# Optimization experiments

Measured on AMD Instinct MI355X. Metric: run time of the kernel, lower is better.

## Reference

```python
import jax, jax.numpy as jnp
import numpy as np
from jax.ops import segment_sum

N_NODES = 50000
N_EDGES = 800000
IN_DIM, HID_DIM, OUT_DIM = 128, 128, 64
N_GRAPHS = 64


def setup_inputs() -> dict:
    key = jax.random.key(0)
    ks = jax.random.split(key, 8)
    x = jax.random.normal(ks[0], (N_NODES, IN_DIM), dtype=jnp.float32)
    edge_index = jax.random.randint(ks[1], (2, N_EDGES), 0, N_NODES, dtype=jnp.int64)
    batch = jnp.sort(jax.random.randint(ks[2], (N_NODES,), 0, N_GRAPHS, dtype=jnp.int64))
    # Glorot-ish init for GCNConv linear weights, zero bias (PyG default)
    W1 = jax.random.normal(ks[3], (IN_DIM, HID_DIM), dtype=jnp.float32) / np.sqrt(IN_DIM)
    b1 = jnp.zeros((HID_DIM,), dtype=jnp.float32)
    W2 = jax.random.normal(ks[4], (HID_DIM, OUT_DIM), dtype=jnp.float32) / np.sqrt(HID_DIM)
    b2 = jnp.zeros((OUT_DIM,), dtype=jnp.float32)
    return {"x": x, "W1": W1, "b1": b1, "W2": W2, "b2": b2,
            "edge_index": edge_index, "batch": batch, "num_graphs": N_GRAPHS}


def _gcn_conv(h, W, b, src, dst, deg_inv_sqrt, n_nodes):
    # h: [N, Fin] -> [N, Fout]; GCNConv: D^{-1/2}(A+I)D^{-1/2} (h W) + b
    hw = h @ W                                   # [N, Fout]
    norm = deg_inv_sqrt[src] * deg_inv_sqrt[dst] # [E]
    msg = hw[src] * norm[:, None]                # [E, Fout] (gather)
    agg = segment_sum(msg, dst, num_segments=n_nodes)  # scatter-add
    # self-loop contribution: norm_ii = deg_inv_sqrt[i]^2
    agg = agg + hw * (deg_inv_sqrt * deg_inv_sqrt)[:, None]
    return agg + b


def reference(x, W1, b1, W2, b2, edge_index, batch, num_graphs):
    n_nodes = x.shape[0]
    src, dst = edge_index[0], edge_index[1]
    # degree of A + I (self-loops added, as in PyG GCNConv default)
    deg = segment_sum(jnp.ones_like(dst, dtype=x.dtype), dst,
                      num_segments=n_nodes) + 1.0
    deg_inv_sqrt = jax.lax.rsqrt(deg)

    h = jax.nn.relu(_gcn_conv(x, W1, b1, src, dst, deg_inv_sqrt, n_nodes))
    h = jax.nn.relu(_gcn_conv(h, W2, b2, src, dst, deg_inv_sqrt, n_nodes))

    # global_mean_pool over batch ids
    sums = segment_sum(h, batch, num_segments=num_graphs)          # [G, Fout]
    counts = segment_sum(jnp.ones((n_nodes,), dtype=h.dtype), batch,
                         num_segments=num_graphs)                  # [G]
    return sums / jnp.maximum(counts, 1.0)[:, None]
```

## Files before the change

### kernel.cpp

```cpp
#include <hip/hip_runtime.h>

typedef float f4 __attribute__((ext_vector_type(4)));
typedef float f2 __attribute__((ext_vector_type(2)));
typedef short s8 __attribute__((ext_vector_type(8)));

union FU { unsigned u[4]; s8 s; };

__device__ __forceinline__ unsigned cvtpk(float lo, float hi){
  unsigned r;
  asm("v_cvt_pk_bf16_f32 %0, %1, %2" : "=v"(r) : "v"(lo), "v"(hi));
  return r;
}

__device__ __forceinline__ float bflo(unsigned v){ return __uint_as_float(v << 16); }
__device__ __forceinline__ float bfhi(unsigned v){ return __uint_as_float(v & 0xFFFF0000u); }

__device__ __forceinline__ int ld_idx(const void* p, int i, int is64){
  if (is64) return (int)((const long long*)p)[i];
  return ((const int*)p)[i];
}

__device__ __forceinline__ int detect64(const unsigned* __restrict__ e_raw, int e){
  int lane = threadIdx.x & 63;
  int lim = (e < 1024) ? e : 1024;
  int nz = 0;
  for (int i = lane; i < lim; i += 64) nz |= (e_raw[2*i + 1] != 0u);
  return (__ballot(nz != 0) == 0ull) ? 1 : 0;
}

template<int NC, int BIN>
__device__ __forceinline__ void gemm_body(const void* __restrict__ Xv,
                                          const float* __restrict__ W,
                                          unsigned short* __restrict__ Yb,
                                          int n, int blk, char* Alds){
  constexpr int NCF = NC/16;
  constexpr int WPC = 8/NCF;
  constexpr int RT  = 8/WPC;
  const int tid  = threadIdx.x;
  const int wave = tid >> 6, lane = tid & 63;
  const int rb = blk * 128;

  const int cbase = (wave % NCF) * 16;
  const int rt0   = (wave / NCF) * RT;
  const int col   = cbase + (lane & 15);
  const int kr0   = (lane >> 4) * 8;
  FU bu[4];
#pragma unroll
  for (int ks = 0; ks < 4; ++ks){
    float wv[8];
#pragma unroll
    for (int j = 0; j < 8; ++j) wv[j] = W[(size_t)(ks*32 + kr0 + j)*NC + col];
#pragma unroll
    for (int q = 0; q < 4; ++q) bu[ks].u[q] = cvtpk(wv[2*q], wv[2*q+1]);
  }

  for (int i = tid; i < 128*32; i += 512){
    int row = i >> 5, kq = i & 31;
    int rsrc = rb + row; if (rsrc >= n) rsrc = n - 1;
    uint2 dw;
    if (BIN){
      dw = ((const uint2*)Xv)[(size_t)rsrc*32 + kq];
    } else {
      f4 xv = ((const f4*)Xv)[(size_t)rsrc*32 + kq];
      dw = make_uint2(cvtpk(xv[0], xv[1]), cvtpk(xv[2], xv[3]));
    }
    int byte = (row*256 + kq*8) ^ ((row & 7) << 4);
    *reinterpret_cast<uint2*>(Alds + byte) = dw;
  }
  __syncthreads();

  f4 acc[RT];
#pragma unroll
  for (int rt = 0; rt < RT; ++rt) acc[rt] = 0.0f;

#pragma unroll
  for (int rt = 0; rt < RT; ++rt){
    const int arow = (rt0 + rt)*16 + (lane & 15);
#pragma unroll
    for (int ks = 0; ks < 4; ++ks){
      int kb = ks*32 + kr0;
      int byte = (arow*256 + kb*2) ^ ((arow & 7) << 4);
      s8 a = *reinterpret_cast<const s8*>(Alds + byte);
      acc[rt] = __builtin_amdgcn_mfma_f32_16x16x32_bf16(a, bu[ks].s, acc[rt], 0, 0, 0);
    }
  }

#pragma unroll
  for (int rt = 0; rt < RT; ++rt){
    int rowb = rb + (rt0 + rt)*16 + 4*(lane >> 4);
#pragma unroll
    for (int r = 0; r < 4; ++r){
      int row = rowb + r;
      if (row < n) Yb[(size_t)row*NC + col] = (unsigned short)cvtpk(acc[rt][r], acc[rt][r]);
    }
  }
}

template<int NC, int BIN>
__global__ __launch_bounds__(512) void gemm_k(const void* __restrict__ X,
                                              const float* __restrict__ W,
                                              unsigned short* __restrict__ Yb, int n){
  __shared__ int4 AldsV[2048];
  gemm_body<NC, BIN>(X, W, Yb, n, blockIdx.x, (char*)AldsV);
}

__global__ __launch_bounds__(512) void fused1_k(const float* __restrict__ X,
                                                const float* __restrict__ W1,
                                                unsigned short* __restrict__ Yb,
                                                const void* __restrict__ eidx,
                                                const void* __restrict__ batchp,
                                                int* __restrict__ counts,
                                                unsigned* __restrict__ etmp,
                                                int* __restrict__ batch32,
                                                int n, int e, int GB, int CB){
  __shared__ int4 AldsV[2048];
  __shared__ int hist[512];
  int blk = blockIdx.x;
  if (blk < GB){
    gemm_body<128, 0>(X, W1, Yb, n, blk, (char*)AldsV);
    return;
  }
  blk -= GB;
  const int NBK = (n + 127) >> 7;
  for (int i = threadIdx.x; i < NBK; i += 512) hist[i] = 0;
  __syncthreads();
  int is64 = detect64((const unsigned*)eidx, e);
  int CHK = (e + CB - 1) / CB;
  int beg = blk*CHK, end = min(e, beg + CHK);
  for (int i = beg + (int)threadIdx.x; i < end; i += 512){
    int s = ld_idx(eidx, i, is64);
    int d = ld_idx(eidx, e + i, is64);
    atomicAdd(&hist[d >> 7], 1);
    etmp[i] = (unsigned)s | ((unsigned)(d & 127) << 16) | ((unsigned)(d >> 7) << 23);
  }
  __syncthreads();
  for (int i = threadIdx.x; i < NBK; i += 512) counts[i*CB + blk] = hist[i];
  for (int i = blk*512 + (int)threadIdx.x; i < n; i += CB*512)
    batch32[i] = ld_idx(batchp, i, is64);
}

__global__ void scanA_k(const int* __restrict__ counts, int* __restrict__ base,
                        int* __restrict__ bsum, int L,
                        float* __restrict__ outsum, int totalOut){
  __shared__ int sh[256];
  int tid = threadIdx.x;
  int i = blockIdx.x*256 + tid;
  int v = (i < L) ? counts[i] : 0;
  sh[tid] = v; __syncthreads();
  for (int off = 1; off < 256; off <<= 1){
    int t = (tid >= off) ? sh[tid - off] : 0;
    __syncthreads();
    sh[tid] += t;
    __syncthreads();
  }
  if (i < L) base[i] = sh[tid] - v;
  if (tid == 255) bsum[blockIdx.x] = sh[255];
  if (blockIdx.x == 0){
    for (int k = tid; k < totalOut; k += 256) outsum[k] = 0.0f;
  }
}

__global__ __launch_bounds__(512) void scat_k(const unsigned* __restrict__ etmp,
                                              const int* __restrict__ base,
                                              const int* __restrict__ bsum,
                                              int* __restrict__ bsumS,
                                              int* __restrict__ packed,
                                              int n, int e, int CB){
  __shared__ int sh[512];
  __shared__ int cur[512];
  int blk = blockIdx.x, tid = threadIdx.x;
  const int NBK = (n + 127) >> 7;
  int v = (tid < NBK) ? bsum[tid] : 0;
  sh[tid] = v; __syncthreads();
  for (int o = 1; o < 512; o <<= 1){
    int t = (tid >= o) ? sh[tid - o] : 0;
    __syncthreads();
    sh[tid] += t;
    __syncthreads();
  }
  int ex = sh[tid] - v;
  if (tid < NBK) cur[tid] = ex + base[tid*CB + blk];
  if (blk == 0){
    if (tid < NBK) bsumS[tid] = ex;
    if (tid == NBK - 1) bsumS[NBK] = sh[tid];
  }
  __syncthreads();
  int CHK = (e + CB - 1) / CB;
  int beg = blk*CHK, end = min(e, beg + CHK);
  for (int i = beg + tid; i < end; i += 512){
    unsigned w = etmp[i];
    int pos = atomicAdd(&cur[w >> 23], 1);
    packed[pos] = (int)(w & 0x7FFFFFu);
  }
}

#define CSR_CAP 6144
__global__ __launch_bounds__(256) void csr_k(const int* __restrict__ packed,
                                             const int* __restrict__ bsumS,
                                             int* __restrict__ esrcS,
                                             int* __restrict__ rowptr,
                                             float* __restrict__ dinv, int n, int e){
  __shared__ int vals[CSR_CAP];
  __shared__ int hist[128], off[128], cur[128];
  int b = blockIdx.x, tid = threadIdx.x;
  if (b == 0 && tid == 0) rowptr[n] = e;
  int sbeg = bsumS[b], send = bsumS[b + 1];
  int m = send - sbeg;
  int mL = min(m, CSR_CAP);
  for (int i = tid; i < mL; i += 256) vals[i] = packed[sbeg + i];
  if (tid < 128) hist[tid] = 0;
  __syncthreads();
  for (int i = tid; i < m; i += 256){
    int v = (i < CSR_CAP) ? vals[i] : packed[sbeg + i];
    atomicAdd(&hist[(v >> 16) & 127], 1);
  }
  __syncthreads();
  if (tid < 128) off[tid] = hist[tid];
  __syncthreads();
  for (int o = 1; o < 128; o <<= 1){
    int v = 0;
    if (tid < 128 && tid >= o) v = off[tid - o];
    __syncthreads();
    if (tid < 128) off[tid] += v;
    __syncthreads();
  }
  if (tid < 128){
    int ex = off[tid] - hist[tid];
    cur[tid] = ex;
    int node = b*128 + tid;
    if (node < n){
      rowptr[node] = sbeg + ex;
      dinv[node] = rsqrtf((float)hist[tid] + 1.0f);
    }
  }
  __syncthreads();
  for (int i = tid; i < m; i += 256){
    int v = (i < CSR_CAP) ? vals[i] : packed[sbeg + i];
    int pos = atomicAdd(&cur[(v >> 16) & 127], 1);
    esrcS[sbeg + pos] = v & 0xFFFF;
  }
}

__global__ __launch_bounds__(256) void agg128_k(const unsigned short* __restrict__ HWb,
                                                const float* __restrict__ dinv,
                                                const int* __restrict__ rowptr,
                                                const int* __restrict__ esrcS,
                                                const float* __restrict__ bias,
                                                unsigned* __restrict__ Hb, int n){
  int wid  = (blockIdx.x*256 + threadIdx.x) >> 6;
  int lane = threadIdx.x & 63;
  if (wid >= n) return;
  wid = __builtin_amdgcn_readfirstlane(wid);
  float di = dinv[wid];
  float di2 = di * di;
  int beg = __builtin_amdgcn_readfirstlane(rowptr[wid]);
  int end = __builtin_amdgcn_readfirstlane(rowptr[wid + 1]);
  unsigned sv = ((const unsigned*)(HWb + (size_t)wid*128))[lane];
  float a0 = bflo(sv) * di2, a1 = bfhi(sv) * di2;
  int j = beg;
  for (; j + 16 <= end; j += 16){
    int s[16]; float dv[16]; unsigned v[16];
#pragma unroll
    for (int t = 0; t < 16; ++t) s[t] = esrcS[j + t];
#pragma unroll
    for (int t = 0; t < 16; ++t){
      dv[t] = dinv[s[t]];
      v[t] = ((const unsigned*)(HWb + (size_t)s[t]*128))[lane];
    }
#pragma unroll
    for (int t = 0; t < 16; ++t){
      float wt = dv[t] * di;
      a0 += bflo(v[t]) * wt;
      a1 += bfhi(v[t]) * wt;
    }
  }
  for (; j + 4 <= end; j += 4){
    int s[4]; float dv[4]; unsigned v[4];
#pragma unroll
    for (int t = 0; t < 4; ++t) s[t] = esrcS[j + t];
#pragma unroll
    for (int t = 0; t < 4; ++t){
      dv[t] = dinv[s[t]];
      v[t] = ((const unsigned*)(HWb + (size_t)s[t]*128))[lane];
    }
#pragma unroll
    for (int t = 0; t < 4; ++t){
      float wt = dv[t] * di;
      a0 += bflo(v[t]) * wt;
      a1 += bfhi(v[t]) * wt;
    }
  }
  for (; j < end; ++j){
    int s = esrcS[j];
    float wt = dinv[s] * di;
    unsigned v = ((const unsigned*)(HWb + (size_t)s*128))[lane];
    a0 += bflo(v) * wt;
    a1 += bfhi(v) * wt;
  }
  f2 bb = ((const f2*)bias)[lane];
  a0 = fmaxf(a0 + bb[0], 0.0f);
  a1 = fmaxf(a1 + bb[1], 0.0f);
  Hb[(size_t)wid*64 + lane] = cvtpk(a0, a1);
}

__global__ __launch_bounds__(256) void agg64_k(const unsigned short* __restrict__ HWb,
                                               const float* __restrict__ dinv,
                                               const int* __restrict__ rowptr,
                                               const int* __restrict__ esrcS,
                                               const float* __restrict__ bias,
                                               float* __restrict__ H2, int n){
  int wid  = (blockIdx.x*256 + threadIdx.x) >> 6;
  int lane = threadIdx.x & 63;
  if (wid >= n) return;
  wid = __builtin_amdgcn_readfirstlane(wid);
  float di = dinv[wid];
  float di2 = di * di;
  int beg = __builtin_amdgcn_readfirstlane(rowptr[wid]);
  int end = __builtin_amdgcn_readfirstlane(rowptr[wid + 1]);
  float acc = bflo((unsigned)HWb[(size_t)wid*64 + lane]) * di2;
  int j = beg;
  for (; j + 16 <= end; j += 16){
    int s[16]; float dv[16]; unsigned v[16];
#pragma unroll
    for (int t = 0; t < 16; ++t) s[t] = esrcS[j + t];
#pragma unroll
    for (int t = 0; t < 16; ++t){
      dv[t] = dinv[s[t]];
      v[t] = (unsigned)HWb[(size_t)s[t]*64 + lane];
    }
#pragma unroll
    for (int t = 0; t < 16; ++t) acc += bflo(v[t]) * (dv[t] * di);
  }
  for (; j + 4 <= end; j += 4){
    int s[4]; float dv[4]; unsigned v[4];
#pragma unroll
    for (int t = 0; t < 4; ++t) s[t] = esrcS[j + t];
#pragma unroll
    for (int t = 0; t < 4; ++t){
      dv[t] = dinv[s[t]];
      v[t] = (unsigned)HWb[(size_t)s[t]*64 + lane];
    }
#pragma unroll
    for (int t = 0; t < 4; ++t) acc += bflo(v[t]) * (dv[t] * di);
  }
  for (; j < end; ++j){
    int s = esrcS[j];
    acc += bflo((unsigned)HWb[(size_t)s*64 + lane]) * (dinv[s] * di);
  }
  acc = fmaxf(acc + bias[lane], 0.0f);
  H2[(size_t)wid*64 + lane] = acc;
}

__global__ __launch_bounds__(256) void pool_k(const float* __restrict__ H2,
                                              const int* __restrict__ batch32,
                                              float* __restrict__ outsum, int n){
  int wid  = (blockIdx.x*256 + threadIdx.x) >> 6;
  int lane = threadIdx.x & 63;
  int start = wid * 8;
  if (start >= n) return;
  int cnt = min(8, n - start);
  float v[8]; int b[8];
#pragma unroll
  for (int t = 0; t < 8; ++t){
    int i = start + t; if (i >= n) i = n - 1;
    v[t] = H2[(size_t)i*64 + lane];
    b[t] = batch32[i];
  }
  float acc = 0.0f;
  int gcur = b[0];
#pragma unroll
  for (int t = 0; t < 8; ++t){
    if (t < cnt){
      if (b[t] != gcur){
        unsafeAtomicAdd(&outsum[gcur*64 + lane], acc);
        acc = 0.0f; gcur = b[t];
      }
      acc += v[t];
    }
  }
  unsafeAtomicAdd(&outsum[gcur*64 + lane], acc);
}

__global__ void fin_k(const float* __restrict__ outsum,
                      const int* __restrict__ batch32,
                      float* __restrict__ out, int n, int g){
  __shared__ int starts[257];
  int t = threadIdx.x;
  if (t <= g){
    int lo = 0, hi = n;
    while (lo < hi){ int mid = (lo + hi) >> 1; if (batch32[mid] < t) lo = mid + 1; else hi = mid; }
    starts[t] = lo;
  }
  __syncthreads();
  for (int idx = t; idx < (g << 6); idx += 256){
    int gi = idx >> 6;
    float c = (float)(starts[gi + 1] - starts[gi]);
    out[idx] = outsum[idx] / fmaxf(c, 1.0f);
  }
}

extern "C" void kernel_launch(void* const* d_in, const int* in_sizes, int n_in,
                              void* d_out, int out_size, void* d_ws, size_t ws_size,
                              hipStream_t stream){
  const float* x    = (const float*)d_in[0];
  const float* W1   = (const float*)d_in[1];
  const float* b1   = (const float*)d_in[2];
  const float* W2   = (const float*)d_in[3];
  const float* b2   = (const float*)d_in[4];
  const void*  eidx = d_in[5];
  const void*  batchp = d_in[6];
  const int n = in_sizes[0] / 128;
  const int e = in_sizes[5] / 2;
  const int g = out_size / 64;
  float* out = (float*)d_out;

  const int NBK = (n + 127) >> 7;
  const int CB  = 256;
  const int GB  = (n + 127) / 128;
  const int L   = NBK * CB;

  char* w = (char*)d_ws;
  int* counts  = (int*)w;
  int* base    = counts + (size_t)L;
  int* bsum    = base + (size_t)L;
  int* bsumS   = bsum + NBK;
  int* rowptr  = bsumS + (NBK + 1);
  int* batch32 = rowptr + (n + 1);
  float* dinv  = (float*)(batch32 + n);
  float* outsum = dinv + n;
  unsigned* etmp = (unsigned*)(outsum + out_size);
  int* packed  = (int*)(etmp + e);
  int* esrcS   = packed + e;
  size_t ofs = (size_t)((char*)(esrcS + e) - w);
  ofs = (ofs + 255) & ~(size_t)255;
  unsigned short* HWb = (unsigned short*)(w + ofs);
  size_t ofs2 = ofs + (size_t)n * 128 * 2;
  ofs2 = (ofs2 + 255) & ~(size_t)255;
  unsigned short* Hb = (unsigned short*)(w + ofs2);
  size_t ofs3 = ofs2 + (size_t)n * 128 * 2;
  ofs3 = (ofs3 + 255) & ~(size_t)255;
  float* H2 = (float*)(w + ofs3);

  fused1_k<<<GB + CB, 512, 0, stream>>>(x, W1, HWb, eidx, batchp,
                                        counts, etmp, batch32, n, e, GB, CB);
  scanA_k<<<NBK, 256, 0, stream>>>(counts, base, bsum, L, outsum, out_size);
  scat_k<<<CB, 512, 0, stream>>>(etmp, base, bsum, bsumS, packed, n, e, CB);
  csr_k<<<NBK, 256, 0, stream>>>(packed, bsumS, esrcS, rowptr, dinv, n, e);

  agg128_k<<<(n + 3)/4, 256, 0, stream>>>(HWb, dinv, rowptr, esrcS, b1,
                                          (unsigned*)Hb, n);
  gemm_k<64, 1><<<GB, 512, 0, stream>>>(Hb, W2, HWb, n);
  agg64_k<<<(n + 3)/4, 256, 0, stream>>>(HWb, dinv, rowptr, esrcS, b2, H2, n);

  int pw = (n + 7)/8;
  pool_k<<<(pw + 3)/4, 256, 0, stream>>>(H2, batch32, outsum, n);
  fin_k<<<1, 256, 0, stream>>>(outsum, batch32, out, n, g);
}
```

Baseline: 120.2 us.

## Vectorize neighbor gathers with per-lane edge slots and fold mean-pool finalize

The aggregation kernels now split each wavefront into edge slots (4 slots of 16 lanes for width 128, 8 slots of 8 lanes for width 64). Each lane loads 16 bytes of a neighbor row, so several edges are gathered at once, and the partial sums are combined with cross-lane shuffles at the end. This replaces narrow per-lane 4- or 2-byte gathers and is meant to increase memory-level parallelism and cut the number of load instructions per edge. Separately, the per-graph inverse counts are computed in scanA_k, and pool_k atomically adds scaled values straight into the output, which removes the fin_k launch and the outsum buffer. The costs are shuffle reductions, idle lanes when degrees are small, and float atomics on the output with a different summation order.

```diff
diff --git a/kernel.cpp b/kernel.cpp
--- a/kernel.cpp
+++ b/kernel.cpp
@@ -141,8 +141,10 @@
 
 __global__ void scanA_k(const int* __restrict__ counts, int* __restrict__ base,
                         int* __restrict__ bsum, int L,
-                        float* __restrict__ outsum, int totalOut){
+                        const int* __restrict__ batch32, float* __restrict__ invc,
+                        float* __restrict__ out, int n, int g){
   __shared__ int sh[256];
+  __shared__ int starts[257];
   int tid = threadIdx.x;
   int i = blockIdx.x*256 + tid;
   int v = (i < L) ? counts[i] : 0;
@@ -156,7 +158,17 @@
   if (i < L) base[i] = sh[tid] - v;
   if (tid == 255) bsum[blockIdx.x] = sh[255];
   if (blockIdx.x == 0){
-    for (int k = tid; k < totalOut; k += 256) outsum[k] = 0.0f;
+    if (tid <= g){
+      int lo = 0, hi = n;
+      while (lo < hi){ int mid = (lo + hi) >> 1; if (batch32[mid] < tid) lo = mid + 1; else hi = mid; }
+      starts[tid] = lo;
+    }
+    __syncthreads();
+    if (tid < g){
+      float c = (float)(starts[tid + 1] - starts[tid]);
+      invc[tid] = 1.0f / fmaxf(c, 1.0f);
+    }
+    for (int k = tid; k < (g << 6); k += 256) out[k] = 0.0f;
   }
 }
 
@@ -246,61 +258,73 @@
                                                 const int* __restrict__ rowptr,
                                                 const int* __restrict__ esrcS,
                                                 const float* __restrict__ bias,
-                                                unsigned* __restrict__ Hb, int n){
+                                                unsigned short* __restrict__ Hb, int n){
   int wid  = (blockIdx.x*256 + threadIdx.x) >> 6;
   int lane = threadIdx.x & 63;
   if (wid >= n) return;
   wid = __builtin_amdgcn_readfirstlane(wid);
+  const int slot = lane >> 4;
+  const int cg   = lane & 15;
   float di = dinv[wid];
   float di2 = di * di;
   int beg = __builtin_amdgcn_readfirstlane(rowptr[wid]);
   int end = __builtin_amdgcn_readfirstlane(rowptr[wid + 1]);
-  unsigned sv = ((const unsigned*)(HWb + (size_t)wid*128))[lane];
-  float a0 = bflo(sv) * di2, a1 = bfhi(sv) * di2;
+  float acc[8];
+#pragma unroll
+  for (int k = 0; k < 8; ++k) acc[k] = 0.0f;
+  const char* Hc = (const char*)HWb;
   int j = beg;
   for (; j + 16 <= end; j += 16){
-    int s[16]; float dv[16]; unsigned v[16];
-#pragma unroll
-    for (int t = 0; t < 16; ++t) s[t] = esrcS[j + t];
-#pragma unroll
-    for (int t = 0; t < 16; ++t){
-      dv[t] = dinv[s[t]];
-      v[t] = ((const unsigned*)(HWb + (size_t)s[t]*128))[lane];
-    }
-#pragma unroll
-    for (int t = 0; t < 16; ++t){
-      float wt = dv[t] * di;
-      a0 += bflo(v[t]) * wt;
-      a1 += bfhi(v[t]) * wt;
-    }
-  }
-  for (; j + 4 <= end; j += 4){
-    int s[4]; float dv[4]; unsigned v[4];
-#pragma unroll
-    for (int t = 0; t < 4; ++t) s[t] = esrcS[j + t];
-#pragma unroll
-    for (int t = 0; t < 4; ++t){
-      dv[t] = dinv[s[t]];
-      v[t] = ((const unsigned*)(HWb + (size_t)s[t]*128))[lane];
-    }
-#pragma unroll
-    for (int t = 0; t < 4; ++t){
-      float wt = dv[t] * di;
-      a0 += bflo(v[t]) * wt;
-      a1 += bfhi(v[t]) * wt;
-    }
-  }
-  for (; j < end; ++j){
-    int s = esrcS[j];
-    float wt = dinv[s] * di;
-    unsigned v = ((const unsigned*)(HWb + (size_t)s*128))[lane];
-    a0 += bflo(v) * wt;
-    a1 += bfhi(v) * wt;
-  }
-  f2 bb = ((const f2*)bias)[lane];
-  a0 = fmaxf(a0 + bb[0], 0.0f);
-  a1 = fmaxf(a1 + bb[1], 0.0f);
-  Hb[(size_t)wid*64 + lane] = cvtpk(a0, a1);
+    int s[4]; float wt[4]; uint4 v[4];
+#pragma unroll
+    for (int q = 0; q < 4; ++q) s[q] = esrcS[j + q*4 + slot];
+#pragma unroll
+    for (int q = 0; q < 4; ++q){
+      wt[q] = dinv[s[q]] * di;
+      v[q] = *(const uint4*)(Hc + (size_t)s[q]*256 + cg*16);
+    }
+#pragma unroll
+    for (int q = 0; q < 4; ++q){
+      acc[0] += bflo(v[q].x)*wt[q]; acc[1] += bfhi(v[q].x)*wt[q];
+      acc[2] += bflo(v[q].y)*wt[q]; acc[3] += bfhi(v[q].y)*wt[q];
+      acc[4] += bflo(v[q].z)*wt[q]; acc[5] += bfhi(v[q].z)*wt[q];
+      acc[6] += bflo(v[q].w)*wt[q]; acc[7] += bfhi(v[q].w)*wt[q];
+    }
+  }
+  for (; j < end; j += 4){
+    int idx = j + slot;
+    int live = (idx < end);
+    if (!live) idx = end - 1;
+    int s = esrcS[idx];
+    float wt = live ? (dinv[s] * di) : 0.0f;
+    uint4 v = *(const uint4*)(Hc + (size_t)s*256 + cg*16);
+    acc[0] += bflo(v.x)*wt; acc[1] += bfhi(v.x)*wt;
+    acc[2] += bflo(v.y)*wt; acc[3] += bfhi(v.y)*wt;
+    acc[4] += bflo(v.z)*wt; acc[5] += bfhi(v.z)*wt;
+    acc[6] += bflo(v.w)*wt; acc[7] += bfhi(v.w)*wt;
+  }
+#pragma unroll
+  for (int k = 0; k < 8; ++k){
+    acc[k] += __shfl_xor(acc[k], 16);
+    acc[k] += __shfl_xor(acc[k], 32);
+  }
+  uint4 sv = *(const uint4*)(Hc + (size_t)wid*256 + cg*16);
+  acc[0] += bflo(sv.x)*di2; acc[1] += bfhi(sv.x)*di2;
+  acc[2] += bflo(sv.y)*di2; acc[3] += bfhi(sv.y)*di2;
+  acc[4] += bflo(sv.z)*di2; acc[5] += bfhi(sv.z)*di2;
+  acc[6] += bflo(sv.w)*di2; acc[7] += bfhi(sv.w)*di2;
+  f4 b0 = *(const f4*)(bias + cg*8);
+  f4 b1 = *(const f4*)(bias + cg*8 + 4);
+#pragma unroll
+  for (int k = 0; k < 4; ++k) acc[k] = fmaxf(acc[k] + b0[k], 0.0f);
+#pragma unroll
+  for (int k = 0; k < 4; ++k) acc[4+k] = fmaxf(acc[4+k] + b1[k], 0.0f);
+  if (slot == 0){
+    uint4 o;
+    o.x = cvtpk(acc[0], acc[1]); o.y = cvtpk(acc[2], acc[3]);
+    o.z = cvtpk(acc[4], acc[5]); o.w = cvtpk(acc[6], acc[7]);
+    *(uint4*)((char*)Hb + (size_t)wid*256 + cg*16) = o;
+  }
 }
 
 __global__ __launch_bounds__(256) void agg64_k(const unsigned short* __restrict__ HWb,
@@ -313,47 +337,75 @@
   int lane = threadIdx.x & 63;
   if (wid >= n) return;
   wid = __builtin_amdgcn_readfirstlane(wid);
+  const int slot = lane >> 3;
+  const int cg   = lane & 7;
   float di = dinv[wid];
   float di2 = di * di;
   int beg = __builtin_amdgcn_readfirstlane(rowptr[wid]);
   int end = __builtin_amdgcn_readfirstlane(rowptr[wid + 1]);
-  float acc = bflo((unsigned)HWb[(size_t)wid*64 + lane]) * di2;
+  float acc[8];
+#pragma unroll
+  for (int k = 0; k < 8; ++k) acc[k] = 0.0f;
+  const char* Hc = (const char*)HWb;
   int j = beg;
   for (; j + 16 <= end; j += 16){
-    int s[16]; float dv[16]; unsigned v[16];
-#pragma unroll
-    for (int t = 0; t < 16; ++t) s[t] = esrcS[j + t];
-#pragma unroll
-    for (int t = 0; t < 16; ++t){
-      dv[t] = dinv[s[t]];
-      v[t] = (unsigned)HWb[(size_t)s[t]*64 + lane];
-    }
-#pragma unroll
-    for (int t = 0; t < 16; ++t) acc += bflo(v[t]) * (dv[t] * di);
-  }
-  for (; j + 4 <= end; j += 4){
-    int s[4]; float dv[4]; unsigned v[4];
-#pragma unroll
-    for (int t = 0; t < 4; ++t) s[t] = esrcS[j + t];
-#pragma unroll
-    for (int t = 0; t < 4; ++t){
-      dv[t] = dinv[s[t]];
-      v[t] = (unsigned)HWb[(size_t)s[t]*64 + lane];
-    }
-#pragma unroll
-    for (int t = 0; t < 4; ++t) acc += bflo(v[t]) * (dv[t] * di);
-  }
-  for (; j < end; ++j){
-    int s = esrcS[j];
-    acc += bflo((unsigned)HWb[(size_t)s*64 + lane]) * (dinv[s] * di);
-  }
-  acc = fmaxf(acc + bias[lane], 0.0f);
-  H2[(size_t)wid*64 + lane] = acc;
+    int s[2]; float wt[2]; uint4 v[2];
+#pragma unroll
+    for (int q = 0; q < 2; ++q) s[q] = esrcS[j + q*8 + slot];
+#pragma unroll
+    for (int q = 0; q < 2; ++q){
+      wt[q] = dinv[s[q]] * di;
+      v[q] = *(const uint4*)(Hc + (size_t)s[q]*128 + cg*16);
+    }
+#pragma unroll
+    for (int q = 0; q < 2; ++q){
+      acc[0] += bflo(v[q].x)*wt[q]; acc[1] += bfhi(v[q].x)*wt[q];
+      acc[2] += bflo(v[q].y)*wt[q]; acc[3] += bfhi(v[q].y)*wt[q];
+      acc[4] += bflo(v[q].z)*wt[q]; acc[5] += bfhi(v[q].z)*wt[q];
+      acc[6] += bflo(v[q].w)*wt[q]; acc[7] += bfhi(v[q].w)*wt[q];
+    }
+  }
+  for (; j < end; j += 8){
+    int idx = j + slot;
+    int live = (idx < end);
+    if (!live) idx = end - 1;
+    int s = esrcS[idx];
+    float wt = live ? (dinv[s] * di) : 0.0f;
+    uint4 v = *(const uint4*)(Hc + (size_t)s*128 + cg*16);
+    acc[0] += bflo(v.x)*wt; acc[1] += bfhi(v.x)*wt;
+    acc[2] += bflo(v.y)*wt; acc[3] += bfhi(v.y)*wt;
+    acc[4] += bflo(v.z)*wt; acc[5] += bfhi(v.z)*wt;
+    acc[6] += bflo(v.w)*wt; acc[7] += bfhi(v.w)*wt;
+  }
+#pragma unroll
+  for (int k = 0; k < 8; ++k){
+    acc[k] += __shfl_xor(acc[k], 8);
+    acc[k] += __shfl_xor(acc[k], 16);
+    acc[k] += __shfl_xor(acc[k], 32);
+  }
+  uint4 sv = *(const uint4*)(Hc + (size_t)wid*128 + cg*16);
+  acc[0] += bflo(sv.x)*di2; acc[1] += bfhi(sv.x)*di2;
+  acc[2] += bflo(sv.y)*di2; acc[3] += bfhi(sv.y)*di2;
+  acc[4] += bflo(sv.z)*di2; acc[5] += bfhi(sv.z)*di2;
+  acc[6] += bflo(sv.w)*di2; acc[7] += bfhi(sv.w)*di2;
+  f4 b0 = *(const f4*)(bias + cg*8);
+  f4 b1 = *(const f4*)(bias + cg*8 + 4);
+#pragma unroll
+  for (int k = 0; k < 4; ++k) acc[k] = fmaxf(acc[k] + b0[k], 0.0f);
+#pragma unroll
+  for (int k = 0; k < 4; ++k) acc[4+k] = fmaxf(acc[4+k] + b1[k], 0.0f);
+  if (slot == 0){
+    f4 o0; o0[0]=acc[0]; o0[1]=acc[1]; o0[2]=acc[2]; o0[3]=acc[3];
+    f4 o1; o1[0]=acc[4]; o1[1]=acc[5]; o1[2]=acc[6]; o1[3]=acc[7];
+    *(f4*)(H2 + (size_t)wid*64 + cg*8)     = o0;
+    *(f4*)(H2 + (size_t)wid*64 + cg*8 + 4) = o1;
+  }
 }
 
 __global__ __launch_bounds__(256) void pool_k(const float* __restrict__ H2,
                                               const int* __restrict__ batch32,
-                                              float* __restrict__ outsum, int n){
+                                              const float* __restrict__ invc,
+                                              float* __restrict__ out, int n){
   int wid  = (blockIdx.x*256 + threadIdx.x) >> 6;
   int lane = threadIdx.x & 63;
   int start = wid * 8;
@@ -372,31 +424,13 @@
   for (int t = 0; t < 8; ++t){
     if (t < cnt){
       if (b[t] != gcur){
-        unsafeAtomicAdd(&outsum[gcur*64 + lane], acc);
+        unsafeAtomicAdd(&out[gcur*64 + lane], acc * invc[gcur]);
         acc = 0.0f; gcur = b[t];
       }
       acc += v[t];
     }
   }
-  unsafeAtomicAdd(&outsum[gcur*64 + lane], acc);
-}
-
-__global__ void fin_k(const float* __restrict__ outsum,
-                      const int* __restrict__ batch32,
-                      float* __restrict__ out, int n, int g){
-  __shared__ int starts[257];
-  int t = threadIdx.x;
-  if (t <= g){
-    int lo = 0, hi = n;
-    while (lo < hi){ int mid = (lo + hi) >> 1; if (batch32[mid] < t) lo = mid + 1; else hi = mid; }
-    starts[t] = lo;
-  }
-  __syncthreads();
-  for (int idx = t; idx < (g << 6); idx += 256){
-    int gi = idx >> 6;
-    float c = (float)(starts[gi + 1] - starts[gi]);
-    out[idx] = outsum[idx] / fmaxf(c, 1.0f);
-  }
+  unsafeAtomicAdd(&out[gcur*64 + lane], acc * invc[gcur]);
 }
 
 extern "C" void kernel_launch(void* const* d_in, const int* in_sizes, int n_in,
@@ -427,8 +461,8 @@
   int* rowptr  = bsumS + (NBK + 1);
   int* batch32 = rowptr + (n + 1);
   float* dinv  = (float*)(batch32 + n);
-  float* outsum = dinv + n;
-  unsigned* etmp = (unsigned*)(outsum + out_size);
+  float* invc  = dinv + n;
+  unsigned* etmp = (unsigned*)(invc + g);
   int* packed  = (int*)(etmp + e);
   int* esrcS   = packed + e;
   size_t ofs = (size_t)((char*)(esrcS + e) - w);
@@ -443,16 +477,14 @@
 
   fused1_k<<<GB + CB, 512, 0, stream>>>(x, W1, HWb, eidx, batchp,
                                         counts, etmp, batch32, n, e, GB, CB);
-  scanA_k<<<NBK, 256, 0, stream>>>(counts, base, bsum, L, outsum, out_size);
+  scanA_k<<<NBK, 256, 0, stream>>>(counts, base, bsum, L, batch32, invc, out, n, g);
   scat_k<<<CB, 512, 0, stream>>>(etmp, base, bsum, bsumS, packed, n, e, CB);
   csr_k<<<NBK, 256, 0, stream>>>(packed, bsumS, esrcS, rowptr, dinv, n, e);
 
-  agg128_k<<<(n + 3)/4, 256, 0, stream>>>(HWb, dinv, rowptr, esrcS, b1,
-                                          (unsigned*)Hb, n);
+  agg128_k<<<(n + 3)/4, 256, 0, stream>>>(HWb, dinv, rowptr, esrcS, b1, Hb, n);
   gemm_k<64, 1><<<GB, 512, 0, stream>>>(Hb, W2, HWb, n);
   agg64_k<<<(n + 3)/4, 256, 0, stream>>>(HWb, dinv, rowptr, esrcS, b2, H2, n);
 
   int pw = (n + 7)/8;
-  pool_k<<<(pw + 3)/4, 256, 0, stream>>>(H2, batch32, outsum, n);
-  fin_k<<<1, 256, 0, stream>>>(outsum, batch32, out, n, g);
-}
+  pool_k<<<(pw + 3)/4, 256, 0, stream>>>(H2, batch32, invc, out, n);
+}
```

New measurement: 116.2 us, median of 2. 3.3% less time.
